# Kernel optimization log

Measured on AMD Instinct MI355X. Metric: run time of the kernel, lower is better.

The kernel has to match this reference:

```python
import jax, jax.numpy as jnp
import numpy as np

B, N, D, E, HEADS, HID = 8, 2048, 768, 4, 12, 3072
CAPF = 0.25
CAP = int(CAPF * N)  # 512 tokens per expert
DH = D // HEADS
EPS = 1e-5  # torch LayerNorm default
SCALE = 0.02


def _nested_masks(dim, n_exp):
    # expert e keeps the first dim // 2**e features (nested experts, MoNE)
    m = np.zeros((n_exp, dim), np.float32)
    for e in range(n_exp):
        m[e, : dim >> e] = 1.0
    return jnp.asarray(m)


def _ln(x, g, b):
    mu = x.mean(-1, keepdims=True)
    var = ((x - mu) ** 2).mean(-1, keepdims=True)
    return (x - mu) * jax.lax.rsqrt(var + EPS) * g + b


def setup_inputs() -> dict:
    key = jax.random.key(0)
    ks = jax.random.split(key, 8)
    return {
        "x": jax.random.normal(ks[0], (B, N, D), jnp.float32),
        "Wr": jax.random.normal(ks[1], (D, E), jnp.float32) * SCALE,
        "ln1_g": jnp.ones((D,), jnp.float32),
        "ln1_b": jnp.zeros((D,), jnp.float32),
        "ln2_g": jnp.ones((D,), jnp.float32),
        "ln2_b": jnp.zeros((D,), jnp.float32),
        "Wqkv": jax.random.normal(ks[2], (D, 3 * D), jnp.float32) * SCALE,
        "Wproj": jax.random.normal(ks[3], (D, D), jnp.float32) * SCALE,
        "bproj": jnp.zeros((D,), jnp.float32),
        "W1": jax.random.normal(ks[4], (D, HID), jnp.float32) * SCALE,
        "b1": jnp.zeros((HID,), jnp.float32),
        "W2": jax.random.normal(ks[5], (HID, D), jnp.float32) * SCALE,
        "b2": jnp.zeros((D,), jnp.float32),
    }


def reference(x, Wr, ln1_g, ln1_b, ln2_g, ln2_b, Wqkv, Wproj, bproj, W1, b1, W2, b2):
    mD = _nested_masks(D, E)[None, :, None, :]    # [1,E,1,D]
    mH = _nested_masks(HID, E)[None, :, None, :]  # [1,E,1,HID]

    # ---- expert-choice router ----
    probs = jax.nn.softmax(x @ Wr, axis=-1)                     # [B,N,E]
    gates, idx = jax.lax.top_k(probs.transpose(0, 2, 1), CAP)   # each [B,E,C]
    dispatch = jax.nn.one_hot(idx, N, dtype=x.dtype)            # [B,E,C,N]
    combine = dispatch * gates[..., None]                       # [B,E,C,N]

    # ---- attention branch (per-expert nested-masked attention) ----
    xn = _ln(x, ln1_g, ln1_b)
    xe = jnp.einsum('becn,bnd->becd', dispatch, xn)             # [B,E,C,D]
    qkv = (xe * mD) @ Wqkv                                      # input-masked linear
    q, k, v = jnp.split(qkv, 3, axis=-1)
    q, k, v = q * mD, k * mD, v * mD                            # nested output masks

    def to_heads(t):
        return t.reshape(B, E, CAP, HEADS, DH).transpose(0, 1, 3, 2, 4)  # [B,E,H,C,dh]

    q, k, v = to_heads(q), to_heads(k), to_heads(v)
    att = jax.nn.softmax(jnp.einsum('behcd,behkd->behck', q, k) * (DH ** -0.5), axis=-1)
    o = jnp.einsum('behck,behkd->behcd', att, v)
    o = o.transpose(0, 1, 3, 2, 4).reshape(B, E, CAP, D)
    ye = ((o @ Wproj) + bproj) * mD                             # masked proj
    x = x + jnp.einsum('becd,becn->bnd', ye, combine)           # combine back

    # ---- MLP branch (per-expert nested-masked MLP) ----
    xn2 = _ln(x, ln2_g, ln2_b)
    xe2 = jnp.einsum('becn,bnd->becd', dispatch, xn2)           # [B,E,C,D]
    h = jax.nn.gelu((((xe2 * mD) @ W1) + b1) * mH)              # [B,E,C,HID]
    y = ((h @ W2) + b2) * mD                                    # [B,E,C,D]
    x = x + jnp.einsum('becd,becn->bnd', y, combine)
    return x
```

## Files before the change

kernel.cpp:

```cpp
#include <hip/hip_runtime.h>
#include <stdint.h>

typedef uint16_t u16;
typedef uint32_t u32;
typedef uint64_t u64;
typedef float f32x4 __attribute__((ext_vector_type(4)));
typedef __bf16 bf16x8 __attribute__((ext_vector_type(8)));

#define DEVI __device__ __forceinline__

struct U4 { u32 a, b, c, d; };

DEVI u16 f2bf(float f) {
    u32 u = __builtin_bit_cast(u32, f);
    return (u16)((u + 0x7FFFu + ((u >> 16) & 1u)) >> 16);
}
DEVI float bf2f(u32 h) { return __builtin_bit_cast(float, h << 16); }
DEVI u32 cvt_pk_bf16(float lo, float hi) {
    u32 r;
    asm("v_cvt_pk_bf16_f32 %0, %1, %2" : "=v"(r) : "v"(lo), "v"(hi));
    return r;
}

DEVI float gelu_f(float x) {
    float u = 0.7978845608028654f * (x + 0.044715f * x * x * x);
    float t = exp2f(u * 2.885390081777927f);
    return x * (1.f - 1.f / (t + 1.f));
}

#define GLOAD_LDS16(gp, lp) \
    __builtin_amdgcn_global_load_lds((const __attribute__((address_space(1))) void*)(gp), \
                                     (__attribute__((address_space(3))) void*)(lp), 16, 0, 0)

struct WtJobs {
    const float* src[4]; u16* dst[4];
    int K[4], N[4], ntx[4], start[5];
};
__global__ __launch_bounds__(256) void wt_all_kernel(WtJobs a) {
    int j = 0;
#pragma unroll
    for (int k = 1; k < 4; k++) if ((int)blockIdx.x >= a.start[k]) j = k;
    const int local = blockIdx.x - a.start[j];
    const int N = a.N[j], K = a.K[j];
    const int n0 = (local % a.ntx[j]) * 32, k0 = (local / a.ntx[j]) * 32;
    const float* __restrict__ src = a.src[j];
    u16* __restrict__ dst = a.dst[j];
    __shared__ float tile[32][33];
    int tx = threadIdx.x & 31, ty = threadIdx.x >> 5;
#pragma unroll
    for (int i = 0; i < 32; i += 8)
        tile[ty + i][tx] = src[(size_t)(k0 + ty + i) * N + n0 + tx];
    __syncthreads();
#pragma unroll
    for (int i = 0; i < 32; i += 8)
        dst[(size_t)(n0 + ty + i) * K + k0 + tx] = f2bf(tile[tx][ty + i]);
}

__global__ __launch_bounds__(256) void routerln_kernel(const float* __restrict__ x,
                                                       const float* __restrict__ Wr,
                                                       const float* __restrict__ gw,
                                                       const float* __restrict__ bw,
                                                       float* __restrict__ probs,
                                                       u16* __restrict__ xn) {
    int wv = threadIdx.x >> 6, lane = threadIdx.x & 63;
    size_t t = (size_t)blockIdx.x * 4 + wv;
    const float4* xr = (const float4*)(x + t * 768);
    const float4* wr4 = (const float4*)Wr;
    float4 v[3]; float s = 0, s2 = 0, a0 = 0, a1 = 0, a2 = 0, a3 = 0;
#pragma unroll
    for (int i = 0; i < 3; i++) {
        int f4 = lane + 64 * i;
        v[i] = xr[f4];
        s += v[i].x + v[i].y + v[i].z + v[i].w;
        s2 += v[i].x * v[i].x + v[i].y * v[i].y + v[i].z * v[i].z + v[i].w * v[i].w;
#pragma unroll
        for (int jj = 0; jj < 4; jj++) {
            float xv = (jj == 0) ? v[i].x : (jj == 1) ? v[i].y : (jj == 2) ? v[i].z : v[i].w;
            float4 w = wr4[f4 * 4 + jj];
            a0 = fmaf(xv, w.x, a0); a1 = fmaf(xv, w.y, a1);
            a2 = fmaf(xv, w.z, a2); a3 = fmaf(xv, w.w, a3);
        }
    }
#pragma unroll
    for (int m = 1; m < 64; m <<= 1) {
        s += __shfl_xor(s, m); s2 += __shfl_xor(s2, m);
        a0 += __shfl_xor(a0, m); a1 += __shfl_xor(a1, m);
        a2 += __shfl_xor(a2, m); a3 += __shfl_xor(a3, m);
    }
    float mx = fmaxf(fmaxf(a0, a1), fmaxf(a2, a3));
    float e0 = expf(a0 - mx), e1 = expf(a1 - mx), e2 = expf(a2 - mx), e3 = expf(a3 - mx);
    float inv = 1.f / (e0 + e1 + e2 + e3);
    if (lane < 4) {
        float pv = (lane == 0) ? e0 : (lane == 1) ? e1 : (lane == 2) ? e2 : e3;
        int b = (int)(t >> 11), n = (int)(t & 2047);
        probs[(size_t)(b * 4 + lane) * 2048 + n] = pv * inv;
    }
    float mu = s * (1.f / 768.f);
    float var = s2 * (1.f / 768.f) - mu * mu;
    float rs = rsqrtf(var + 1e-5f);
    uint2* op = (uint2*)(xn + t * 768);
#pragma unroll
    for (int i = 0; i < 3; i++) {
        int j4 = (lane + 64 * i) * 4;
        float y0 = (v[i].x - mu) * rs * gw[j4 + 0] + bw[j4 + 0];
        float y1 = (v[i].y - mu) * rs * gw[j4 + 1] + bw[j4 + 1];
        float y2 = (v[i].z - mu) * rs * gw[j4 + 2] + bw[j4 + 2];
        float y3 = (v[i].w - mu) * rs * gw[j4 + 3] + bw[j4 + 3];
        uint2 o; o.x = cvt_pk_bf16(y0, y1); o.y = cvt_pk_bf16(y2, y3);
        op[lane + 64 * i] = o;
    }
}

__global__ __launch_bounds__(1024) void topk_kernel(const float* __restrict__ probs,
                                                    int* __restrict__ idx, float* __restrict__ gate,
                                                    int* __restrict__ rev) {
    int be = blockIdx.x; int b = be >> 2, e = be & 3;
    __shared__ u64 keys[2048];
    for (int n = threadIdx.x; n < 2048; n += 1024) {
        u32 p = __builtin_bit_cast(u32, probs[(size_t)be * 2048 + n]);
        keys[n] = ((u64)p << 32) | (u32)(2047 - n);
        rev[((size_t)b * 2048 + n) * 4 + e] = -1;
    }
    __syncthreads();
    for (int k = 2; k <= 2048; k <<= 1)
        for (int j = k >> 1; j > 0; j >>= 1) {
            for (int i = threadIdx.x; i < 2048; i += 1024) {
                int ixj = i ^ j;
                if (ixj > i) {
                    u64 a = keys[i], bb = keys[ixj];
                    bool up = ((i & k) == 0);
                    if (up ? (a < bb) : (a > bb)) { keys[i] = bb; keys[ixj] = a; }
                }
            }
            __syncthreads();
        }
    for (int c = threadIdx.x; c < 512; c += 1024) {
        u64 kk = keys[c];
        int n = 2047 - (int)(kk & 0xffffffffu);
        idx[be * 512 + c] = n;
        gate[be * 512 + c] = __builtin_bit_cast(float, (u32)(kk >> 32));
        rev[((size_t)b * 2048 + n) * 4 + e] = c;
    }
}

struct GemmJobs {
    const u16* A[4]; u16* C[4]; u16* VT[4]; const int* idx[4];
    const u16* BT; const float* bias;
    long sAb[4], sCb[4], sVb[4];
    int lda[4], ldc[4], nk[4], nmask[4], tps[4], tstart[4];
    int ldb;
};

template <int MODE>
__global__ __launch_bounds__(256) void gemm_kernel(GemmJobs a) {
    __shared__ __align__(16) char smem[2][16384];
    const int tid = threadIdx.x, wv = tid >> 6, lane = tid & 63;
    const int bid = blockIdx.x;
    const int bz = bid & 7;
    const int mt = (bid >> 3) & 3;
    const int sidx = bid >> 5;
    int e = 0;
#pragma unroll
    for (int k = 1; k < 4; k++) if (sidx >= a.tstart[k]) e = k;
    const int local = sidx - a.tstart[e];
    int seg, ntl;
    if (MODE == 0) { seg = local / a.tps[e]; ntl = local - seg * a.tps[e]; }
    else { seg = 0; ntl = local; }
    const int nbase = seg * 768 + ntl * 128;
    const int lda = a.lda[e], ldc = a.ldc[e], nk = a.nk[e], nmask = a.nmask[e];
    const u16* Ap = a.A[e] + (long)bz * a.sAb[e];
    const int* ix = a.idx[e] ? (a.idx[e] + bz * 2048) : nullptr;
    const bool swapped = (MODE != 0) || (seg < 2);

    auto stage = [&](int buf, int kt) {
        char* base = smem[buf] + ((wv >= 2) ? 8192 : 0);
        const int kb = kt * 32;
#pragma unroll
        for (int q = 0; q < 4; q++) {
            int i8 = (wv & 1) * 4 + q;
            int row = i8 * 16 + (lane >> 2);
            int clog = ((lane & 3) * 16) ^ ((row & 6) << 3);
            const u16* g;
            if (wv < 2) {
                int rs = ix ? ix[mt * 128 + row] : (mt * 128 + row);
                g = Ap + (long)rs * lda + kb;
            } else {
                g = a.BT + (long)(nbase + row) * a.ldb + kb;
            }
            GLOAD_LDS16((const char*)g + clog, base + i8 * 1024);
        }
    };

    f32x4 acc[4][4] = {};
    stage(0, 0);
    __syncthreads();
    int buf = 0;
    const int wr = wv >> 1, wc = wv & 1;
    const int l15 = lane & 15, lg = lane >> 4;
    const int cb = lg * 16;
    for (int kt = 0; kt < nk; kt++) {
        if (kt + 1 < nk) stage(buf ^ 1, kt + 1);
        const char* ab = smem[buf];
        const char* bb = smem[buf] + 8192;
        bf16x8 af[4], bfv[4];
#pragma unroll
        for (int mi = 0; mi < 4; mi++) {
            int r = wr * 64 + mi * 16 + l15;
            af[mi] = *(const bf16x8*)(ab + r * 64 + (cb ^ ((r & 6) << 3)));
        }
#pragma unroll
        for (int ni = 0; ni < 4; ni++) {
            int r = wc * 64 + ni * 16 + l15;
            bfv[ni] = *(const bf16x8*)(bb + r * 64 + (cb ^ ((r & 6) << 3)));
        }
        if (swapped) {
#pragma unroll
            for (int mi = 0; mi < 4; mi++)
#pragma unroll
                for (int ni = 0; ni < 4; ni++)
                    acc[mi][ni] = __builtin_amdgcn_mfma_f32_16x16x32_bf16(bfv[ni], af[mi], acc[mi][ni], 0, 0, 0);
        } else {
#pragma unroll
            for (int mi = 0; mi < 4; mi++)
#pragma unroll
                for (int ni = 0; ni < 4; ni++)
                    acc[mi][ni] = __builtin_amdgcn_mfma_f32_16x16x32_bf16(af[mi], bfv[ni], acc[mi][ni], 0, 0, 0);
        }
        __syncthreads();
        buf ^= 1;
    }

    u16* Cb = a.C[e] + (long)bz * a.sCb[e];
    if (MODE == 0 && seg == 2) {
        u16* Vb = a.VT[e] + (long)bz * a.sVb[e];
#pragma unroll
        for (int mi = 0; mi < 4; mi++) {
            const int r0 = mt * 128 + wr * 64 + mi * 16 + (lg << 2);
#pragma unroll
            for (int ni = 0; ni < 4; ni++) {
                const int nloc = ntl * 128 + wc * 64 + ni * 16 + l15;
                const bool act = nloc < nmask;
                uint2 pv;
                if (act) { pv.x = cvt_pk_bf16(acc[mi][ni][0], acc[mi][ni][1]);
                           pv.y = cvt_pk_bf16(acc[mi][ni][2], acc[mi][ni][3]); }
                else { pv.x = 0; pv.y = 0; }
                *(uint2*)(Vb + (long)nloc * 512 + r0) = pv;
            }
        }
    } else if (MODE == 0) {
#pragma unroll
        for (int mi = 0; mi < 4; mi++) {
            const int row = mt * 128 + wr * 64 + mi * 16 + l15;
            u16* cp = Cb + (long)row * 1536 + seg * 768 + ntl * 128;
#pragma unroll
            for (int ni = 0; ni < 4; ni++) {
                const int colb = wc * 64 + ni * 16 + lg * 4;
                const bool act = (ntl * 128 + colb) < nmask;
                uint2 pv;
                if (act) { pv.x = cvt_pk_bf16(acc[mi][ni][0], acc[mi][ni][1]);
                           pv.y = cvt_pk_bf16(acc[mi][ni][2], acc[mi][ni][3]); }
                else { pv.x = 0; pv.y = 0; }
                *(uint2*)(cp + colb) = pv;
            }
        }
    } else {
#pragma unroll
        for (int mi = 0; mi < 4; mi++) {
            const int row = mt * 128 + wr * 64 + mi * 16 + l15;
#pragma unroll
            for (int ni = 0; ni < 4; ni++) {
                const int nloc = ntl * 128 + wc * 64 + ni * 16 + lg * 4;
                const float4 bv = *(const float4*)(a.bias + nloc);
                float v0 = acc[mi][ni][0] + bv.x, v1 = acc[mi][ni][1] + bv.y;
                float v2 = acc[mi][ni][2] + bv.z, v3 = acc[mi][ni][3] + bv.w;
                if (MODE == 2) { v0 = gelu_f(v0); v1 = gelu_f(v1); v2 = gelu_f(v2); v3 = gelu_f(v3); }
                uint2 pv; pv.x = cvt_pk_bf16(v0, v1); pv.y = cvt_pk_bf16(v2, v3);
                *(uint2*)(Cb + (long)row * ldc + nloc) = pv;
            }
        }
    }
}

__global__ __launch_bounds__(256) void attn_kernel(const u16* __restrict__ qkv,
                                                   const u16* __restrict__ vt,
                                                   u16* __restrict__ obuf) {
    const int bid = blockIdx.x;
    const int jobl = bid % 184;
    const int qt = bid / 184;
    const int b = jobl / 23, hj = jobl % 23;
    int e, h;
    if (hj < 12) { e = 0; h = hj; }
    else if (hj < 18) { e = 1; h = hj - 12; }
    else if (hj < 21) { e = 2; h = hj - 18; }
    else { e = 3; h = hj - 21; }
    const int job = b * 4 + e;
    const u16* qkvj = qkv + (size_t)job * 512 * 1536;
    const u16* vtj = vt + (size_t)job * 768 * 512 + (size_t)h * 64 * 512;
    u16* oj = obuf + (size_t)job * 512 * 768;
    __shared__ __align__(16) char lds[16384];
    const int tid = threadIdx.x, wv = tid >> 6;
    const int lane = tid & 63, l15 = lane & 15, lg = lane >> 4;
    const int q0 = qt * 128 + wv * 32;

    bf16x8 qf[2][2];
#pragma unroll
    for (int n2 = 0; n2 < 2; n2++)
#pragma unroll
        for (int ks = 0; ks < 2; ks++)
            qf[n2][ks] = *(const bf16x8*)(qkvj + (size_t)(q0 + n2 * 16 + l15) * 1536 + h * 64 + ks * 32 + lg * 8);

    f32x4 oacc[4][2] = {};
    float mrun[2] = {-1e30f, -1e30f}, lrun[2] = {0.f, 0.f};
    const float SA = 0.18033688011112042f;

    for (int t = 0; t < 4; t++) {
        const int kv0 = t * 128;

        f32x4 sacc[8][2] = {};
#pragma unroll
        for (int ks = 0; ks < 2; ks++)
#pragma unroll
            for (int m8 = 0; m8 < 8; m8++) {
                bf16x8 kf = *(const bf16x8*)(qkvj + (size_t)(kv0 + m8 * 16 + l15) * 1536 + 768 + h * 64 + ks * 32 + lg * 8);
#pragma unroll
                for (int n2 = 0; n2 < 2; n2++)
                    sacc[m8][n2] = __builtin_amdgcn_mfma_f32_16x16x32_bf16(kf, qf[n2][ks], sacc[m8][n2], 0, 0, 0);
            }

        u32 pk[8][2][2];
#pragma unroll
        for (int n2 = 0; n2 < 2; n2++) {
            float pm[8];
#pragma unroll
            for (int m8 = 0; m8 < 8; m8++)
                pm[m8] = fmaxf(fmaxf(sacc[m8][n2][0], sacc[m8][n2][1]),
                               fmaxf(sacc[m8][n2][2], sacc[m8][n2][3]));
            float tm = fmaxf(fmaxf(fmaxf(pm[0], pm[1]), fmaxf(pm[2], pm[3])),
                             fmaxf(fmaxf(pm[4], pm[5]), fmaxf(pm[6], pm[7])));
            tm = fmaxf(tm, __shfl_xor(tm, 16));
            tm = fmaxf(tm, __shfl_xor(tm, 32));
            float mnew = fmaxf(mrun[n2], tm);
            float alpha = exp2f((mrun[n2] - mnew) * SA);
            float ps[8];
#pragma unroll
            for (int m8 = 0; m8 < 8; m8++) {
#pragma unroll
                for (int j = 0; j < 4; j++)
                    sacc[m8][n2][j] = exp2f((sacc[m8][n2][j] - mnew) * SA);
                ps[m8] = (sacc[m8][n2][0] + sacc[m8][n2][1]) + (sacc[m8][n2][2] + sacc[m8][n2][3]);
            }
            float tsum = ((ps[0] + ps[1]) + (ps[2] + ps[3])) + ((ps[4] + ps[5]) + (ps[6] + ps[7]));
            tsum += __shfl_xor(tsum, 16);
            tsum += __shfl_xor(tsum, 32);
            lrun[n2] = lrun[n2] * alpha + tsum;
            mrun[n2] = mnew;
#pragma unroll
            for (int mo = 0; mo < 4; mo++) oacc[mo][n2] *= alpha;
#pragma unroll
            for (int m8 = 0; m8 < 8; m8++) {
                pk[m8][n2][0] = cvt_pk_bf16(sacc[m8][n2][0], sacc[m8][n2][1]);
                pk[m8][n2][1] = cvt_pk_bf16(sacc[m8][n2][2], sacc[m8][n2][3]);
            }
        }

        const int la = ((2 * lg) & 3) * 16 + l15;
        const int lb = ((2 * lg + 1) & 3) * 16 + l15;
#pragma unroll
        for (int kb = 0; kb < 4; kb++) {
            bf16x8 pb[2];
#pragma unroll
            for (int n2 = 0; n2 < 2; n2++) {
                u32 w[4];
#pragma unroll
                for (int half = 0; half < 2; half++) {
                    int src = (half == 0) ? la : lb;
                    u32 aA = (u32)__shfl((int)pk[2 * kb + 0][n2][0], src);
                    u32 aB = (u32)__shfl((int)pk[2 * kb + 1][n2][0], src);
                    u32 bA = (u32)__shfl((int)pk[2 * kb + 0][n2][1], src);
                    u32 bB = (u32)__shfl((int)pk[2 * kb + 1][n2][1], src);
                    w[half * 2 + 0] = (lg < 2) ? aA : aB;
                    w[half * 2 + 1] = (lg < 2) ? bA : bB;
                }
                U4 uw{w[0], w[1], w[2], w[3]};
                pb[n2] = __builtin_bit_cast(bf16x8, uw);
            }
#pragma unroll
            for (int mo = 0; mo < 4; mo++) {
                bf16x8 vf = *(const bf16x8*)(vtj + (size_t)(mo * 16 + l15) * 512 + kv0 + kb * 32 + lg * 8);
#pragma unroll
                for (int n2 = 0; n2 < 2; n2++)
                    oacc[mo][n2] = __builtin_amdgcn_mfma_f32_16x16x32_bf16(vf, pb[n2], oacc[mo][n2], 0, 0, 0);
            }
        }
    }

    char* Wl = lds + wv * 4096;
#pragma unroll
    for (int n2 = 0; n2 < 2; n2++) {
        float inv = 1.f / lrun[n2];
        int c = n2 * 16 + l15;
#pragma unroll
        for (int mo = 0; mo < 4; mo++) {
            int tch = mo * 2 + (lg >> 1);
            int byteoff = c * 128 + (((tch ^ (c & 7)) << 4)) + (lg & 1) * 8;
            uint2 o;
            o.x = cvt_pk_bf16(oacc[mo][n2][0] * inv, oacc[mo][n2][1] * inv);
            o.y = cvt_pk_bf16(oacc[mo][n2][2] * inv, oacc[mo][n2][3] * inv);
            *(uint2*)(Wl + byteoff) = o;
        }
    }
    asm volatile("s_waitcnt lgkmcnt(0)" ::: "memory");
    __builtin_amdgcn_sched_barrier(0);
#pragma unroll
    for (int p = 0; p < 4; p++) {
        int row = p * 8 + (lane >> 3);
        int tch = lane & 7;
        uint4 v = *(const uint4*)(Wl + row * 128 + ((tch ^ (row & 7)) << 4));
        *(uint4*)(oj + (size_t)(q0 + row) * 768 + h * 64 + tch * 8) = v;
    }
}

template <int DO_LN>
__global__ __launch_bounds__(256) void combineln_kernel(const float* __restrict__ basex,
                                                        float* __restrict__ outp,
                                                        const u16* __restrict__ ye,
                                                        const int* __restrict__ rev,
                                                        const float* __restrict__ gate,
                                                        const float* __restrict__ gw,
                                                        const float* __restrict__ bw,
                                                        u16* __restrict__ xn) {
    int wv = threadIdx.x >> 6, lane = threadIdx.x & 63;
    size_t t = (size_t)blockIdx.x * 4 + wv;
    const int b = (int)(t >> 11);
    const int4 rv = *(const int4*)(rev + t * 4);
    const int cs[4] = {rv.x, rv.y, rv.z, rv.w};
    float4 v[3];
#pragma unroll
    for (int i = 0; i < 3; i++) v[i] = *(const float4*)(basex + t * 768 + (lane + 64 * i) * 4);
#pragma unroll
    for (int e = 0; e < 4; e++) {
        const int c = cs[e];
        if (c >= 0) {
            const int job = b * 4 + e;
            const float g = gate[job * 512 + c];
            const u16* yr = ye + ((size_t)job * 512 + c) * 768;
#pragma unroll
            for (int i = 0; i < 3; i++) {
                int f4 = lane + 64 * i;
                if (f4 < (192 >> e)) {
                    uint2 raw = *(const uint2*)(yr + f4 * 4);
                    v[i].x += g * bf2f(raw.x & 0xffffu);
                    v[i].y += g * bf2f(raw.x >> 16);
                    v[i].z += g * bf2f(raw.y & 0xffffu);
                    v[i].w += g * bf2f(raw.y >> 16);
                }
            }
        }
    }
#pragma unroll
    for (int i = 0; i < 3; i++) *(float4*)(outp + t * 768 + (lane + 64 * i) * 4) = v[i];
    if (DO_LN) {
        float s = 0, s2 = 0;
#pragma unroll
        for (int i = 0; i < 3; i++) {
            s += v[i].x + v[i].y + v[i].z + v[i].w;
            s2 += v[i].x * v[i].x + v[i].y * v[i].y + v[i].z * v[i].z + v[i].w * v[i].w;
        }
#pragma unroll
        for (int m = 1; m < 64; m <<= 1) { s += __shfl_xor(s, m); s2 += __shfl_xor(s2, m); }
        float mu = s * (1.f / 768.f);
        float var = s2 * (1.f / 768.f) - mu * mu;
        float rs = rsqrtf(var + 1e-5f);
        uint2* op = (uint2*)(xn + t * 768);
#pragma unroll
        for (int i = 0; i < 3; i++) {
            int j4 = (lane + 64 * i) * 4;
            float y0 = (v[i].x - mu) * rs * gw[j4 + 0] + bw[j4 + 0];
            float y1 = (v[i].y - mu) * rs * gw[j4 + 1] + bw[j4 + 1];
            float y2 = (v[i].z - mu) * rs * gw[j4 + 2] + bw[j4 + 2];
            float y3 = (v[i].w - mu) * rs * gw[j4 + 3] + bw[j4 + 3];
            uint2 o; o.x = cvt_pk_bf16(y0, y1); o.y = cvt_pk_bf16(y2, y3);
            op[lane + 64 * i] = o;
        }
    }
}

extern "C" void kernel_launch(void* const* d_in, const int* in_sizes, int n_in,
                              void* d_out, int out_size, void* d_ws, size_t ws_size,
                              hipStream_t stream) {
    (void)in_sizes; (void)n_in; (void)out_size; (void)ws_size;
    const float* x     = (const float*)d_in[0];
    const float* Wr    = (const float*)d_in[1];
    const float* ln1g  = (const float*)d_in[2];
    const float* ln1b  = (const float*)d_in[3];
    const float* ln2g  = (const float*)d_in[4];
    const float* ln2b  = (const float*)d_in[5];
    const float* Wqkv  = (const float*)d_in[6];
    const float* Wproj = (const float*)d_in[7];
    const float* bproj = (const float*)d_in[8];
    const float* W1    = (const float*)d_in[9];
    const float* b1    = (const float*)d_in[10];
    const float* W2    = (const float*)d_in[11];
    const float* b2    = (const float*)d_in[12];
    float* outp = (float*)d_out;

    char* ws = (char*)d_ws;
    size_t off = 0;
    auto take = [&](size_t bytes) -> void* {
        void* p = ws + off;
        off += (bytes + 255) & ~(size_t)255;
        return p;
    };
    u16*   WqkvT  = (u16*)take((size_t)2304 * 768 * 2);
    u16*   WprojT = (u16*)take((size_t)768 * 768 * 2);
    u16*   W1T    = (u16*)take((size_t)3072 * 768 * 2);
    u16*   W2T    = (u16*)take((size_t)768 * 3072 * 2);
    float* probs  = (float*)take((size_t)32 * 2048 * 4);
    int*   idxb   = (int*)take((size_t)32 * 512 * 4);
    float* gateb  = (float*)take((size_t)32 * 512 * 4);
    int*   revb   = (int*)take((size_t)8 * 2048 * 4 * 4);
    u16*   xn     = (u16*)take((size_t)8 * 2048 * 768 * 2);
    u16*   qkvb   = (u16*)take((size_t)32 * 512 * 1536 * 2);
    u16*   vtb    = (u16*)take((size_t)32 * 768 * 512 * 2);
    u16*   ob     = (u16*)take((size_t)32 * 512 * 768 * 2);
    u16*   yeb    = (u16*)take((size_t)32 * 512 * 768 * 2);
    u16*   hb     = qkvb;

    const int Dk_[4] = {768, 384, 192, 96};
    const int He_[4] = {3072, 1536, 768, 384};
    size_t eoffH[4];
    { size_t s = 0; for (int e = 0; e < 4; e++) { eoffH[e] = s; s += (size_t)8 * 512 * He_[e]; } }

    WtJobs wj{};
    wj.src[0] = Wqkv;  wj.dst[0] = WqkvT;  wj.K[0] = 768;  wj.N[0] = 2304;
    wj.src[1] = Wproj; wj.dst[1] = WprojT; wj.K[1] = 768;  wj.N[1] = 768;
    wj.src[2] = W1;    wj.dst[2] = W1T;    wj.K[2] = 768;  wj.N[2] = 3072;
    wj.src[3] = W2;    wj.dst[3] = W2T;    wj.K[3] = 3072; wj.N[3] = 768;
    { int s = 0; for (int j = 0; j < 4; j++) { wj.ntx[j] = wj.N[j] / 32; wj.start[j] = s; s += (wj.N[j] / 32) * (wj.K[j] / 32); } wj.start[4] = s;
      wt_all_kernel<<<s, 256, 0, stream>>>(wj); }

    routerln_kernel<<<4096, 256, 0, stream>>>(x, Wr, ln1g, ln1b, probs, xn);
    topk_kernel<<<32, 1024, 0, stream>>>(probs, idxb, gateb, revb);

    {
        GemmJobs ga{};
        ga.BT = WqkvT; ga.bias = nullptr; ga.ldb = 768;
        int s = 0;
        for (int e = 0; e < 4; e++) {
            int tps = (Dk_[e] + 127) / 128;
            ga.A[e] = xn; ga.C[e] = qkvb + (size_t)e * 512 * 1536; ga.VT[e] = vtb + (size_t)e * 768 * 512;
            ga.idx[e] = idxb + e * 512;
            ga.sAb[e] = (long)2048 * 768; ga.sCb[e] = (long)4 * 512 * 1536; ga.sVb[e] = (long)4 * 768 * 512;
            ga.lda[e] = 768; ga.ldc[e] = 1536; ga.nk[e] = Dk_[e] / 32; ga.nmask[e] = Dk_[e];
            ga.tps[e] = tps; ga.tstart[e] = s; s += 3 * tps;
        }
        gemm_kernel<0><<<s * 32, 256, 0, stream>>>(ga);
    }

    attn_kernel<<<736, 256, 0, stream>>>(qkvb, vtb, ob);

    {
        GemmJobs ga{};
        ga.BT = WprojT; ga.bias = bproj; ga.ldb = 768;
        int s = 0;
        for (int e = 0; e < 4; e++) {
            int tps = (Dk_[e] + 127) / 128;
            ga.A[e] = ob + (size_t)e * 512 * 768; ga.C[e] = yeb + (size_t)e * 512 * 768;
            ga.VT[e] = nullptr; ga.idx[e] = nullptr;
            ga.sAb[e] = (long)4 * 512 * 768; ga.sCb[e] = (long)4 * 512 * 768; ga.sVb[e] = 0;
            ga.lda[e] = 768; ga.ldc[e] = 768; ga.nk[e] = Dk_[e] / 32; ga.nmask[e] = 768;
            ga.tps[e] = tps; ga.tstart[e] = s; s += tps;
        }
        gemm_kernel<1><<<s * 32, 256, 0, stream>>>(ga);
    }

    combineln_kernel<1><<<4096, 256, 0, stream>>>(x, outp, yeb, revb, gateb, ln2g, ln2b, xn);

    {
        GemmJobs ga{};
        ga.BT = W1T; ga.bias = b1; ga.ldb = 768;
        int s = 0;
        for (int e = 0; e < 4; e++) {
            ga.A[e] = xn; ga.C[e] = hb + eoffH[e]; ga.VT[e] = nullptr; ga.idx[e] = idxb + e * 512;
            ga.sAb[e] = (long)2048 * 768; ga.sCb[e] = (long)512 * He_[e]; ga.sVb[e] = 0;
            ga.lda[e] = 768; ga.ldc[e] = He_[e]; ga.nk[e] = Dk_[e] / 32; ga.nmask[e] = He_[e];
            ga.tps[e] = He_[e] / 128; ga.tstart[e] = s; s += He_[e] / 128;
        }
        gemm_kernel<2><<<s * 32, 256, 0, stream>>>(ga);
    }
    {
        GemmJobs ga{};
        ga.BT = W2T; ga.bias = b2; ga.ldb = 3072;
        int s = 0;
        for (int e = 0; e < 4; e++) {
            int tps = (Dk_[e] + 127) / 128;
            ga.A[e] = hb + eoffH[e]; ga.C[e] = yeb + (size_t)e * 512 * 768;
            ga.VT[e] = nullptr; ga.idx[e] = nullptr;
            ga.sAb[e] = (long)512 * He_[e]; ga.sCb[e] = (long)4 * 512 * 768; ga.sVb[e] = 0;
            ga.lda[e] = He_[e]; ga.ldc[e] = 768; ga.nk[e] = He_[e] / 32; ga.nmask[e] = 768;
            ga.tps[e] = tps; ga.tstart[e] = s; s += tps;
        }
        gemm_kernel<1><<<s * 32, 256, 0, stream>>>(ga);
    }

    combineln_kernel<0><<<4096, 256, 0, stream>>>(outp, outp, yeb, revb, gateb, nullptr, nullptr, nullptr);
}
```

Measured before the change: 509.7 us.

## Stage K/V tiles in shared LDS and use 8 waves of 16 queries in attention

The attention kernel now cooperatively loads each 128-key K tile and the matching V^T tile into swizzled LDS, and all waves read their MFMA operands from there instead of each wave fetching them separately from global memory. The block grows to 512 threads, with each wave handling 16 query rows instead of 32. This is meant to cut redundant global/L2 traffic and raise latency hiding through more waves. The cost is two __syncthreads per KV tile, twice the LDS per block, and fewer MFMAs per wave, which may lower issue efficiency.

```diff
diff --git a/kernel.cpp b/kernel.cpp
--- a/kernel.cpp
+++ b/kernel.cpp
@@ -281,7 +281,7 @@
     }
 }
 
-__global__ __launch_bounds__(256) void attn_kernel(const u16* __restrict__ qkv,
+__global__ __launch_bounds__(512) void attn_kernel(const u16* __restrict__ qkv,
                                                    const u16* __restrict__ vt,
                                                    u16* __restrict__ obuf) {
     const int bid = blockIdx.x;
@@ -297,122 +297,121 @@
     const u16* qkvj = qkv + (size_t)job * 512 * 1536;
     const u16* vtj = vt + (size_t)job * 768 * 512 + (size_t)h * 64 * 512;
     u16* oj = obuf + (size_t)job * 512 * 768;
-    __shared__ __align__(16) char lds[16384];
+    __shared__ __align__(16) char lds[32768];
+    char* Klds = lds;
+    char* Vlds = lds + 16384;
     const int tid = threadIdx.x, wv = tid >> 6;
     const int lane = tid & 63, l15 = lane & 15, lg = lane >> 4;
-    const int q0 = qt * 128 + wv * 32;
-
-    bf16x8 qf[2][2];
-#pragma unroll
-    for (int n2 = 0; n2 < 2; n2++)
-#pragma unroll
-        for (int ks = 0; ks < 2; ks++)
-            qf[n2][ks] = *(const bf16x8*)(qkvj + (size_t)(q0 + n2 * 16 + l15) * 1536 + h * 64 + ks * 32 + lg * 8);
-
-    f32x4 oacc[4][2] = {};
-    float mrun[2] = {-1e30f, -1e30f}, lrun[2] = {0.f, 0.f};
+    const int q0 = qt * 128 + wv * 16;
+
+    bf16x8 qf[2];
+#pragma unroll
+    for (int ks = 0; ks < 2; ks++)
+        qf[ks] = *(const bf16x8*)(qkvj + (size_t)(q0 + l15) * 1536 + h * 64 + ks * 32 + lg * 8);
+
+    f32x4 oacc[4] = {};
+    float mrun = -1e30f, lrun = 0.f;
     const float SA = 0.18033688011112042f;
+    const int la = ((2 * lg) & 3) * 16 + l15;
+    const int lb = ((2 * lg + 1) & 3) * 16 + l15;
 
     for (int t = 0; t < 4; t++) {
         const int kv0 = t * 128;
-
-        f32x4 sacc[8][2] = {};
+        __syncthreads();
+#pragma unroll
+        for (int ii = 0; ii < 2; ii++) {
+            int kslot = tid + 512 * ii;
+            int kr = kslot >> 3, kc = kslot & 7;
+            *(uint4*)(Klds + kr * 128 + ((kc ^ (kr & 7)) << 4)) =
+                *(const uint4*)(qkvj + (size_t)(kv0 + kr) * 1536 + 768 + h * 64 + kc * 8);
+            int vr = kslot >> 4, vc = kslot & 15;
+            *(uint4*)(Vlds + vr * 256 + ((vc ^ (vr & 7)) << 4)) =
+                *(const uint4*)(vtj + (size_t)vr * 512 + kv0 + vc * 8);
+        }
+        __syncthreads();
+
+        f32x4 sacc[8] = {};
 #pragma unroll
         for (int ks = 0; ks < 2; ks++)
 #pragma unroll
             for (int m8 = 0; m8 < 8; m8++) {
-                bf16x8 kf = *(const bf16x8*)(qkvj + (size_t)(kv0 + m8 * 16 + l15) * 1536 + 768 + h * 64 + ks * 32 + lg * 8);
-#pragma unroll
-                for (int n2 = 0; n2 < 2; n2++)
-                    sacc[m8][n2] = __builtin_amdgcn_mfma_f32_16x16x32_bf16(kf, qf[n2][ks], sacc[m8][n2], 0, 0, 0);
-            }
-
-        u32 pk[8][2][2];
-#pragma unroll
-        for (int n2 = 0; n2 < 2; n2++) {
-            float pm[8];
-#pragma unroll
-            for (int m8 = 0; m8 < 8; m8++)
-                pm[m8] = fmaxf(fmaxf(sacc[m8][n2][0], sacc[m8][n2][1]),
-                               fmaxf(sacc[m8][n2][2], sacc[m8][n2][3]));
-            float tm = fmaxf(fmaxf(fmaxf(pm[0], pm[1]), fmaxf(pm[2], pm[3])),
-                             fmaxf(fmaxf(pm[4], pm[5]), fmaxf(pm[6], pm[7])));
-            tm = fmaxf(tm, __shfl_xor(tm, 16));
-            tm = fmaxf(tm, __shfl_xor(tm, 32));
-            float mnew = fmaxf(mrun[n2], tm);
-            float alpha = exp2f((mrun[n2] - mnew) * SA);
-            float ps[8];
-#pragma unroll
-            for (int m8 = 0; m8 < 8; m8++) {
-#pragma unroll
-                for (int j = 0; j < 4; j++)
-                    sacc[m8][n2][j] = exp2f((sacc[m8][n2][j] - mnew) * SA);
-                ps[m8] = (sacc[m8][n2][0] + sacc[m8][n2][1]) + (sacc[m8][n2][2] + sacc[m8][n2][3]);
-            }
-            float tsum = ((ps[0] + ps[1]) + (ps[2] + ps[3])) + ((ps[4] + ps[5]) + (ps[6] + ps[7]));
-            tsum += __shfl_xor(tsum, 16);
-            tsum += __shfl_xor(tsum, 32);
-            lrun[n2] = lrun[n2] * alpha + tsum;
-            mrun[n2] = mnew;
-#pragma unroll
-            for (int mo = 0; mo < 4; mo++) oacc[mo][n2] *= alpha;
-#pragma unroll
-            for (int m8 = 0; m8 < 8; m8++) {
-                pk[m8][n2][0] = cvt_pk_bf16(sacc[m8][n2][0], sacc[m8][n2][1]);
-                pk[m8][n2][1] = cvt_pk_bf16(sacc[m8][n2][2], sacc[m8][n2][3]);
-            }
-        }
-
-        const int la = ((2 * lg) & 3) * 16 + l15;
-        const int lb = ((2 * lg + 1) & 3) * 16 + l15;
+                int r = m8 * 16 + l15;
+                bf16x8 kf = *(const bf16x8*)(Klds + r * 128 + ((ks * 64 + lg * 16) ^ ((r & 7) << 4)));
+                sacc[m8] = __builtin_amdgcn_mfma_f32_16x16x32_bf16(kf, qf[ks], sacc[m8], 0, 0, 0);
+            }
+
+        float pm[8];
+#pragma unroll
+        for (int m8 = 0; m8 < 8; m8++)
+            pm[m8] = fmaxf(fmaxf(sacc[m8][0], sacc[m8][1]), fmaxf(sacc[m8][2], sacc[m8][3]));
+        float tm = fmaxf(fmaxf(fmaxf(pm[0], pm[1]), fmaxf(pm[2], pm[3])),
+                         fmaxf(fmaxf(pm[4], pm[5]), fmaxf(pm[6], pm[7])));
+        tm = fmaxf(tm, __shfl_xor(tm, 16));
+        tm = fmaxf(tm, __shfl_xor(tm, 32));
+        float mnew = fmaxf(mrun, tm);
+        float alpha = exp2f((mrun - mnew) * SA);
+        float ps[8];
+        u32 pk[8][2];
+#pragma unroll
+        for (int m8 = 0; m8 < 8; m8++) {
+#pragma unroll
+            for (int j = 0; j < 4; j++)
+                sacc[m8][j] = exp2f((sacc[m8][j] - mnew) * SA);
+            ps[m8] = (sacc[m8][0] + sacc[m8][1]) + (sacc[m8][2] + sacc[m8][3]);
+            pk[m8][0] = cvt_pk_bf16(sacc[m8][0], sacc[m8][1]);
+            pk[m8][1] = cvt_pk_bf16(sacc[m8][2], sacc[m8][3]);
+        }
+        float tsum = ((ps[0] + ps[1]) + (ps[2] + ps[3])) + ((ps[4] + ps[5]) + (ps[6] + ps[7]));
+        tsum += __shfl_xor(tsum, 16);
+        tsum += __shfl_xor(tsum, 32);
+        lrun = lrun * alpha + tsum;
+        mrun = mnew;
+#pragma unroll
+        for (int mo = 0; mo < 4; mo++) oacc[mo] *= alpha;
+
 #pragma unroll
         for (int kb = 0; kb < 4; kb++) {
-            bf16x8 pb[2];
-#pragma unroll
-            for (int n2 = 0; n2 < 2; n2++) {
-                u32 w[4];
-#pragma unroll
-                for (int half = 0; half < 2; half++) {
-                    int src = (half == 0) ? la : lb;
-                    u32 aA = (u32)__shfl((int)pk[2 * kb + 0][n2][0], src);
-                    u32 aB = (u32)__shfl((int)pk[2 * kb + 1][n2][0], src);
-                    u32 bA = (u32)__shfl((int)pk[2 * kb + 0][n2][1], src);
-                    u32 bB = (u32)__shfl((int)pk[2 * kb + 1][n2][1], src);
-                    w[half * 2 + 0] = (lg < 2) ? aA : aB;
-                    w[half * 2 + 1] = (lg < 2) ? bA : bB;
-                }
-                U4 uw{w[0], w[1], w[2], w[3]};
-                pb[n2] = __builtin_bit_cast(bf16x8, uw);
-            }
+            u32 w[4];
+#pragma unroll
+            for (int half = 0; half < 2; half++) {
+                int src = (half == 0) ? la : lb;
+                u32 aA = (u32)__shfl((int)pk[2 * kb + 0][0], src);
+                u32 aB = (u32)__shfl((int)pk[2 * kb + 1][0], src);
+                u32 bA = (u32)__shfl((int)pk[2 * kb + 0][1], src);
+                u32 bB = (u32)__shfl((int)pk[2 * kb + 1][1], src);
+                w[half * 2 + 0] = (lg < 2) ? aA : aB;
+                w[half * 2 + 1] = (lg < 2) ? bA : bB;
+            }
+            U4 uw{w[0], w[1], w[2], w[3]};
+            bf16x8 pb = __builtin_bit_cast(bf16x8, uw);
 #pragma unroll
             for (int mo = 0; mo < 4; mo++) {
-                bf16x8 vf = *(const bf16x8*)(vtj + (size_t)(mo * 16 + l15) * 512 + kv0 + kb * 32 + lg * 8);
-#pragma unroll
-                for (int n2 = 0; n2 < 2; n2++)
-                    oacc[mo][n2] = __builtin_amdgcn_mfma_f32_16x16x32_bf16(vf, pb[n2], oacc[mo][n2], 0, 0, 0);
-            }
-        }
-    }
-
-    char* Wl = lds + wv * 4096;
-#pragma unroll
-    for (int n2 = 0; n2 < 2; n2++) {
-        float inv = 1.f / lrun[n2];
-        int c = n2 * 16 + l15;
+                int r = mo * 16 + l15;
+                bf16x8 vf = *(const bf16x8*)(Vlds + r * 256 + ((kb * 64 + lg * 16) ^ ((r & 7) << 4)));
+                oacc[mo] = __builtin_amdgcn_mfma_f32_16x16x32_bf16(vf, pb, oacc[mo], 0, 0, 0);
+            }
+        }
+    }
+
+    __syncthreads();
+    char* Wl = lds + wv * 2048;
+    {
+        float inv = 1.f / lrun;
+        int c = l15;
 #pragma unroll
         for (int mo = 0; mo < 4; mo++) {
             int tch = mo * 2 + (lg >> 1);
             int byteoff = c * 128 + (((tch ^ (c & 7)) << 4)) + (lg & 1) * 8;
             uint2 o;
-            o.x = cvt_pk_bf16(oacc[mo][n2][0] * inv, oacc[mo][n2][1] * inv);
-            o.y = cvt_pk_bf16(oacc[mo][n2][2] * inv, oacc[mo][n2][3] * inv);
+            o.x = cvt_pk_bf16(oacc[mo][0] * inv, oacc[mo][1] * inv);
+            o.y = cvt_pk_bf16(oacc[mo][2] * inv, oacc[mo][3] * inv);
             *(uint2*)(Wl + byteoff) = o;
         }
     }
     asm volatile("s_waitcnt lgkmcnt(0)" ::: "memory");
     __builtin_amdgcn_sched_barrier(0);
 #pragma unroll
-    for (int p = 0; p < 4; p++) {
+    for (int p = 0; p < 2; p++) {
         int row = p * 8 + (lane >> 3);
         int tch = lane & 7;
         uint4 v = *(const uint4*)(Wl + row * 128 + ((tch ^ (row & 7)) << 4));
@@ -557,7 +556,7 @@
         gemm_kernel<0><<<s * 32, 256, 0, stream>>>(ga);
     }
 
-    attn_kernel<<<736, 256, 0, stream>>>(qkvb, vtb, ob);
+    attn_kernel<<<736, 512, 0, stream>>>(qkvb, vtb, ob);
 
     {
         GemmJobs ga{};
```

Measured after the change: 450.0 us. 11.7% less time.
